# Performance work log

Hardware: AMD Instinct MI355X
Metric: run time of the kernel (lower is better)

## Reference

```python
import jax, jax.numpy as jnp
import numpy as np


def setup_inputs() -> dict:
    key = jax.random.key(0)
    k1, k2, k3, k4 = jax.random.split(key, 4)
    B, C, H, W = 4, 256, 48, 48
    scale = 1.0 / np.sqrt(C)  # conv-like init scale
    x = jax.random.normal(k1, (B, C, H, W), dtype=jnp.float32)
    wq = jax.random.normal(k2, (C, C), dtype=jnp.float32) * scale
    wk = jax.random.normal(k3, (C, C), dtype=jnp.float32) * scale
    wv = jax.random.normal(k4, (C, C), dtype=jnp.float32) * scale
    return {"x": x, "wq": wq, "wk": wk, "wv": wv}


def reference(x, wq, wk, wv):
    B, C, H, W = x.shape
    num_heads = 8
    d_k = C // num_heads
    N = H * W

    # 1x1 convs (bias=False) are channel-mixing matmuls: [out_c, in_c]
    def proj(w):
        y = jnp.einsum('oc,bchw->bohw', w, x)
        # view(B, heads, d_k, H*W)
        return y.reshape(B, num_heads, d_k, N)

    q = proj(wq)  # [B, h, d_k, N]
    k = proj(wk)
    v = proj(wv)

    # scores = q^T k / sqrt(d_k) -> [B, h, N, N]
    scores = jnp.einsum('bhdn,bhdm->bhnm', q, k) / jnp.sqrt(jnp.asarray(d_k, x.dtype))
    attn = jax.nn.softmax(scores, axis=-1)
    # out = attn @ v^T -> [B, h, N, d_k]
    out = jnp.einsum('bhnm,bhdm->bhnd', attn, v)
    # permute back to [B, h, d_k, N] then view(B, C, H, W)
    out = out.transpose(0, 1, 3, 2).reshape(B, C, H, W)
    return x + out
```

## Files before the change

### kernel.cpp

```cpp
#include <hip/hip_runtime.h>

constexpr int B  = 4;
constexpr int C  = 256;
constexpr int N  = 2304;
constexpr int NH = 8;
constexpr int DK = 32;

typedef short short8 __attribute__((ext_vector_type(8)));
typedef float f32x4  __attribute__((ext_vector_type(4)));

static __device__ __forceinline__ ushort f2bf(float f) {
    union { float f; unsigned u; } v; v.f = f;
    return (ushort)((v.u + 0x7FFFu + ((v.u >> 16) & 1u)) >> 16);
}
static __device__ __forceinline__ unsigned cvtpk(float lo, float hi) {
    unsigned r;
    asm("v_cvt_pk_bf16_f32 %0, %1, %2" : "=v"(r) : "v"(lo), "v"(hi));
    return r;
}

__global__ __launch_bounds__(256) void proj_kernel(
    const float* __restrict__ x,
    const float* __restrict__ wq,
    const float* __restrict__ wk,
    const float* __restrict__ wv,
    ushort* __restrict__ ws,
    int bfix, size_t matStride, size_t batchStride)
{
    const int mat = blockIdx.y;
    const int b   = (bfix >= 0) ? bfix : (int)blockIdx.z;
    const int n0  = (blockIdx.x % 18) * 128;
    const int o0  = (blockIdx.x / 18) * 128;

    const float* w = (mat == 0) ? wq : (mat == 1) ? wk : wv;
    ushort* out = ws + (size_t)mat * matStride + (size_t)b * batchStride;
    const float* xb = x + (size_t)b * C * N;

    __shared__ float xs[16][128];
    __shared__ float wtT[16][132];

    const int tid = threadIdx.x;
    const int tx = tid >> 4;
    const int ty = tid & 15;

    float acc[8][8] = {};

    for (int k0 = 0; k0 < C; k0 += 16) {
        {
            const int kk  = tid >> 4;
            const int nn4 = tid & 15;
            *reinterpret_cast<float4*>(&xs[kk][nn4 * 4]) =
                *reinterpret_cast<const float4*>(xb + (size_t)(k0 + kk) * N + n0 + nn4 * 4);
            *reinterpret_cast<float4*>(&xs[kk][64 + nn4 * 4]) =
                *reinterpret_cast<const float4*>(xb + (size_t)(k0 + kk) * N + n0 + 64 + nn4 * 4);
        }
        {
            const int oo = tid >> 1;
            const int kh = tid & 1;
            float4 wa = *reinterpret_cast<const float4*>(w + (size_t)(o0 + oo) * C + k0 + kh * 4);
            float4 wb = *reinterpret_cast<const float4*>(w + (size_t)(o0 + oo) * C + k0 + kh * 4 + 8);
            wtT[kh * 4 + 0][oo] = wa.x;
            wtT[kh * 4 + 1][oo] = wa.y;
            wtT[kh * 4 + 2][oo] = wa.z;
            wtT[kh * 4 + 3][oo] = wa.w;
            wtT[kh * 4 + 8][oo] = wb.x;
            wtT[kh * 4 + 9][oo] = wb.y;
            wtT[kh * 4 + 10][oo] = wb.z;
            wtT[kh * 4 + 11][oo] = wb.w;
        }
        __syncthreads();

        #pragma unroll
        for (int kk = 0; kk < 16; ++kk) {
            float4 a0 = *reinterpret_cast<const float4*>(&xs[kk][tx * 8]);
            float4 a1 = *reinterpret_cast<const float4*>(&xs[kk][tx * 8 + 4]);
            float4 b0 = *reinterpret_cast<const float4*>(&wtT[kk][ty * 8]);
            float4 b1 = *reinterpret_cast<const float4*>(&wtT[kk][ty * 8 + 4]);
            float av[8] = {a0.x, a0.y, a0.z, a0.w, a1.x, a1.y, a1.z, a1.w};
            float bv[8] = {b0.x, b0.y, b0.z, b0.w, b1.x, b1.y, b1.z, b1.w};
            #pragma unroll
            for (int jn = 0; jn < 8; ++jn)
                #pragma unroll
                for (int jo = 0; jo < 8; ++jo)
                    acc[jn][jo] = fmaf(av[jn], bv[jo], acc[jn][jo]);
        }
        __syncthreads();
    }

    const float sc = (mat == 0) ? 0.25503450535f : 1.0f;
    #pragma unroll
    for (int jn = 0; jn < 8; ++jn) {
        unsigned pk[4];
        #pragma unroll
        for (int p = 0; p < 4; ++p)
            pk[p] = cvtpk(acc[jn][2 * p] * sc, acc[jn][2 * p + 1] * sc);
        *reinterpret_cast<uint4*>(out + (size_t)(n0 + tx * 8 + jn) * C + o0 + ty * 8) =
            make_uint4(pk[0], pk[1], pk[2], pk[3]);
    }
}

__global__ __launch_bounds__(128) void attn_kernel(
    const ushort* __restrict__ ws,
    const float* __restrict__ x,
    float* __restrict__ out,
    int bfix, size_t matStride, size_t batchStride, int ppx)
{
    __shared__ __align__(16) char smem[14336];
    ushort* Ks  = (ushort*)smem;
    ushort* Vt  = (ushort*)(smem + 5120);
    float*  Ost = (float*) smem;

    const int tid = threadIdx.x;
    const int wq  = tid >> 6;
    const int l   = tid & 63;
    const int lq  = l & 15;
    const int g   = l >> 4;

    ushort* Pl = (ushort*)(smem + 9728) + wq * 1152;

    const int gid  = blockIdx.x;
    const int xcd  = gid & 7;
    const int loc  = gid >> 3;
    const int pair = xcd * ppx + loc / 72;
    const int qt   = loc % 72;
    const int h    = pair & 7;
    const int b    = (bfix >= 0) ? bfix : (pair >> 3);
    const int n0   = qt * 32;

    const ushort* qb = ws + (size_t)b * batchStride;
    const ushort* kb = qb + matStride;
    const ushort* vb = qb + 2 * matStride;

    short8 qf = *reinterpret_cast<const short8*>(
        qb + (size_t)(n0 + wq * 16 + lq) * C + h * DK + 8 * g);

    f32x4 acc0 = {0.f, 0.f, 0.f, 0.f};
    f32x4 acc1 = {0.f, 0.f, 0.f, 0.f};
    float m = -1e30f, lsum = 0.f;

    const int kr = tid >> 2, kc = tid & 3;
    const int vp = tid & 31, vd = tid >> 5;

    short8  kreg0, kreg1;
    ushort4 va0, vc0, va1, vc1;

    #define LOAD_TILE(m0_)                                                          \
        {                                                                           \
            const int m0i = (m0_);                                                  \
            kreg0 = *reinterpret_cast<const short8*>(kb + (size_t)(m0i + kr) * C + h * DK + kc * 8);        \
            kreg1 = *reinterpret_cast<const short8*>(kb + (size_t)(m0i + 32 + kr) * C + h * DK + kc * 8);   \
            const ushort* v0 = vb + (size_t)(m0i + 2 * vp) * C + h * DK + vd * 4;   \
            va0 = *reinterpret_cast<const ushort4*>(v0);                            \
            vc0 = *reinterpret_cast<const ushort4*>(v0 + C);                        \
            va1 = *reinterpret_cast<const ushort4*>(v0 + 16);                       \
            vc1 = *reinterpret_cast<const ushort4*>(v0 + C + 16);                   \
        }

    LOAD_TILE(0);

    for (int t = 0; t < N / 64; ++t) {
        *reinterpret_cast<short8*>(Ks + kr * 40 + kc * 8) = kreg0;
        *reinterpret_cast<short8*>(Ks + (kr + 32) * 40 + kc * 8) = kreg1;
        {
            unsigned p0 = (unsigned)va0.x | ((unsigned)vc0.x << 16);
            unsigned p1 = (unsigned)va0.y | ((unsigned)vc0.y << 16);
            unsigned p2 = (unsigned)va0.z | ((unsigned)vc0.z << 16);
            unsigned p3 = (unsigned)va0.w | ((unsigned)vc0.w << 16);
            *reinterpret_cast<unsigned*>(Vt + (vd * 4 + 0) * 72 + 2 * vp) = p0;
            *reinterpret_cast<unsigned*>(Vt + (vd * 4 + 1) * 72 + 2 * vp) = p1;
            *reinterpret_cast<unsigned*>(Vt + (vd * 4 + 2) * 72 + 2 * vp) = p2;
            *reinterpret_cast<unsigned*>(Vt + (vd * 4 + 3) * 72 + 2 * vp) = p3;
            unsigned q0 = (unsigned)va1.x | ((unsigned)vc1.x << 16);
            unsigned q1 = (unsigned)va1.y | ((unsigned)vc1.y << 16);
            unsigned q2 = (unsigned)va1.z | ((unsigned)vc1.z << 16);
            unsigned q3 = (unsigned)va1.w | ((unsigned)vc1.w << 16);
            *reinterpret_cast<unsigned*>(Vt + (vd * 4 + 16) * 72 + 2 * vp) = q0;
            *reinterpret_cast<unsigned*>(Vt + (vd * 4 + 17) * 72 + 2 * vp) = q1;
            *reinterpret_cast<unsigned*>(Vt + (vd * 4 + 18) * 72 + 2 * vp) = q2;
            *reinterpret_cast<unsigned*>(Vt + (vd * 4 + 19) * 72 + 2 * vp) = q3;
        }
        __syncthreads();

        if (t < N / 64 - 1) LOAD_TILE((t + 1) * 64);

        f32x4 st[4];
        __builtin_amdgcn_s_setprio(1);
        #pragma unroll
        for (int u = 0; u < 4; ++u) {
            short8 kf = *reinterpret_cast<const short8*>(Ks + (lq + 16 * u) * 40 + 8 * g);
            f32x4 z = {0.f, 0.f, 0.f, 0.f};
            st[u] = __builtin_amdgcn_mfma_f32_16x16x32_bf16(kf, qf, z, 0, 0, 0);
        }
        __builtin_amdgcn_s_setprio(0);

        float mxl = st[0][0];
        #pragma unroll
        for (int u = 0; u < 4; ++u)
            #pragma unroll
            for (int r = 0; r < 4; ++r) mxl = fmaxf(mxl, st[u][r]);

        if (!__all(mxl <= m + 8.0f)) {
            float mx = fmaxf(mxl, __shfl_xor(mxl, 16));
            mx = fmaxf(mx, __shfl_xor(mx, 32));
            float nm = fmaxf(m, mx);
            float corr = exp2f(m - nm);
            m = nm;
            lsum *= corr;
            float cw0 = __shfl(corr, 4 * g + 0);
            float cw1 = __shfl(corr, 4 * g + 1);
            float cw2 = __shfl(corr, 4 * g + 2);
            float cw3 = __shfl(corr, 4 * g + 3);
            acc0[0] *= cw0; acc0[1] *= cw1; acc0[2] *= cw2; acc0[3] *= cw3;
            acc1[0] *= cw0; acc1[1] *= cw1; acc1[2] *= cw2; acc1[3] *= cw3;
        }

        float ps = 0.f;
        uint2 pw[4];
        #pragma unroll
        for (int u = 0; u < 4; ++u) {
            float p0 = exp2f(st[u][0] - m);
            float p1 = exp2f(st[u][1] - m);
            float p2 = exp2f(st[u][2] - m);
            float p3 = exp2f(st[u][3] - m);
            ps += (p0 + p1) + (p2 + p3);
            pw[u].x = cvtpk(p0, p1);
            pw[u].y = cvtpk(p2, p3);
        }
        lsum += ps;

        #pragma unroll
        for (int u = 0; u < 4; ++u)
            *reinterpret_cast<uint2*>(Pl + lq * 72 + 4 * g + 16 * u) = pw[u];

        short8 pf0 = *reinterpret_cast<const short8*>(Pl + lq * 72 + 8 * g);
        short8 pf1 = *reinterpret_cast<const short8*>(Pl + lq * 72 + 32 + 8 * g);
        __builtin_amdgcn_s_setprio(1);
        #pragma unroll
        for (int k2 = 0; k2 < 2; ++k2) {
            short8 pf = k2 ? pf1 : pf0;
            short8 vf0 = *reinterpret_cast<const short8*>(Vt + lq * 72 + 32 * k2 + 8 * g);
            short8 vf1 = *reinterpret_cast<const short8*>(Vt + (lq + 16) * 72 + 32 * k2 + 8 * g);
            acc0 = __builtin_amdgcn_mfma_f32_16x16x32_bf16(pf, vf0, acc0, 0, 0, 0);
            acc1 = __builtin_amdgcn_mfma_f32_16x16x32_bf16(pf, vf1, acc1, 0, 0, 0);
        }
        __builtin_amdgcn_s_setprio(0);
        __syncthreads();
    }

    lsum += __shfl_xor(lsum, 16);
    lsum += __shfl_xor(lsum, 32);
    const float iv = 1.0f / lsum;
    float iw0 = __shfl(iv, 4 * g + 0);
    float iw1 = __shfl(iv, 4 * g + 1);
    float iw2 = __shfl(iv, 4 * g + 2);
    float iw3 = __shfl(iv, 4 * g + 3);

    Ost[(lq +  0) * 36 + wq * 16 + 4 * g + 0] = acc0[0] * iw0;
    Ost[(lq +  0) * 36 + wq * 16 + 4 * g + 1] = acc0[1] * iw1;
    Ost[(lq +  0) * 36 + wq * 16 + 4 * g + 2] = acc0[2] * iw2;
    Ost[(lq +  0) * 36 + wq * 16 + 4 * g + 3] = acc0[3] * iw3;
    Ost[(lq + 16) * 36 + wq * 16 + 4 * g + 0] = acc1[0] * iw0;
    Ost[(lq + 16) * 36 + wq * 16 + 4 * g + 1] = acc1[1] * iw1;
    Ost[(lq + 16) * 36 + wq * 16 + 4 * g + 2] = acc1[2] * iw2;
    Ost[(lq + 16) * 36 + wq * 16 + 4 * g + 3] = acc1[3] * iw3;
    __syncthreads();

    {
        const int d  = tid >> 2;
        const int nn = (tid & 3) * 8;
        const size_t go = ((size_t)b * C + h * DK + d) * (size_t)N + n0 + nn;
        float4 o1 = *reinterpret_cast<float4*>(Ost + d * 36 + nn);
        float4 o2 = *reinterpret_cast<float4*>(Ost + d * 36 + nn + 4);
        float4 x1 = *reinterpret_cast<const float4*>(x + go);
        float4 x2 = *reinterpret_cast<const float4*>(x + go + 4);
        *reinterpret_cast<float4*>(out + go)     = make_float4(o1.x + x1.x, o1.y + x1.y, o1.z + x1.z, o1.w + x1.w);
        *reinterpret_cast<float4*>(out + go + 4) = make_float4(o2.x + x2.x, o2.y + x2.y, o2.z + x2.z, o2.w + x2.w);
    }
}

extern "C" void kernel_launch(void* const* d_in, const int* in_sizes, int n_in,
                              void* d_out, int out_size, void* d_ws, size_t ws_size,
                              hipStream_t stream) {
    const float* x  = (const float*)d_in[0];
    const float* wq = (const float*)d_in[1];
    const float* wk = (const float*)d_in[2];
    const float* wv = (const float*)d_in[3];
    float* out = (float*)d_out;
    ushort* ws = (ushort*)d_ws;

    const size_t NC = (size_t)N * C;
    const size_t needFull = 3 * (size_t)B * NC * sizeof(ushort);

    if (ws_size >= needFull) {
        proj_kernel<<<dim3(18 * 2, 3, B), 256, 0, stream>>>(
            x, wq, wk, wv, ws, -1, (size_t)B * NC, NC);
        attn_kernel<<<dim3(72 * NH * B), 128, 0, stream>>>(
            ws, x, out, -1, (size_t)B * NC, NC, 4);
    } else {
        for (int b = 0; b < B; ++b) {
            proj_kernel<<<dim3(18 * 2, 3, 1), 256, 0, stream>>>(
                x, wq, wk, wv, ws, b, NC, 0);
            attn_kernel<<<dim3(72 * NH), 128, 0, stream>>>(
                ws, x, out, b, NC, 0, 1);
        }
    }
}
```

Measured before the change: 221.3 us.

## Enlarge attention query tile to 128 rows with 8-wave blocks sharing K/V tiles

The attention kernel now runs 512-thread blocks covering 128 queries instead of 128-thread blocks covering 32. Each K/V tile staged in shared memory is therefore reused by four times as many queries, which cuts global and L2 load traffic and per-query staging work. K loading and V loading/transposing are split between the two halves of the block. In exchange, shared memory per block grows, 8-wave barriers are costlier, and the grid shrinks to 576 blocks, which may leave load imbalance across CUs.

```diff
diff --git a/kernel.cpp b/kernel.cpp
--- a/kernel.cpp
+++ b/kernel.cpp
@@ -9,10 +9,6 @@
 typedef short short8 __attribute__((ext_vector_type(8)));
 typedef float f32x4  __attribute__((ext_vector_type(4)));
 
-static __device__ __forceinline__ ushort f2bf(float f) {
-    union { float f; unsigned u; } v; v.f = f;
-    return (ushort)((v.u + 0x7FFFu + ((v.u >> 16) & 1u)) >> 16);
-}
 static __device__ __forceinline__ unsigned cvtpk(float lo, float hi) {
     unsigned r;
     asm("v_cvt_pk_bf16_f32 %0, %1, %2" : "=v"(r) : "v"(lo), "v"(hi));
@@ -99,13 +95,13 @@
     }
 }
 
-__global__ __launch_bounds__(128) void attn_kernel(
+__global__ __launch_bounds__(512) void attn_kernel(
     const ushort* __restrict__ ws,
     const float* __restrict__ x,
     float* __restrict__ out,
     int bfix, size_t matStride, size_t batchStride, int ppx)
 {
-    __shared__ __align__(16) char smem[14336];
+    __shared__ __align__(16) char smem[28160];
     ushort* Ks  = (ushort*)smem;
     ushort* Vt  = (ushort*)(smem + 5120);
     float*  Ost = (float*) smem;
@@ -121,11 +117,11 @@
     const int gid  = blockIdx.x;
     const int xcd  = gid & 7;
     const int loc  = gid >> 3;
-    const int pair = xcd * ppx + loc / 72;
-    const int qt   = loc % 72;
+    const int pair = xcd * ppx + loc / 18;
+    const int qt   = loc % 18;
     const int h    = pair & 7;
     const int b    = (bfix >= 0) ? bfix : (pair >> 3);
-    const int n0   = qt * 32;
+    const int n0   = qt * 128;
 
     const ushort* qb = ws + (size_t)b * batchStride;
     const ushort* kb = qb + matStride;
@@ -139,45 +135,33 @@
     float m = -1e30f, lsum = 0.f;
 
     const int kr = tid >> 2, kc = tid & 3;
-    const int vp = tid & 31, vd = tid >> 5;
-
-    short8  kreg0, kreg1;
-    ushort4 va0, vc0, va1, vc1;
-
-    #define LOAD_TILE(m0_)                                                          \
-        {                                                                           \
-            const int m0i = (m0_);                                                  \
-            kreg0 = *reinterpret_cast<const short8*>(kb + (size_t)(m0i + kr) * C + h * DK + kc * 8);        \
-            kreg1 = *reinterpret_cast<const short8*>(kb + (size_t)(m0i + 32 + kr) * C + h * DK + kc * 8);   \
+    const int t2 = tid - 256;
+    const int vp = t2 & 31, vd = t2 >> 5;
+
+    short8  kreg;
+    ushort4 va, vc;
+
+    #define LOAD_TILE(m0_) {                                                        \
+        const int m0i = (m0_);                                                      \
+        if (tid < 256) {                                                            \
+            kreg = *reinterpret_cast<const short8*>(kb + (size_t)(m0i + kr) * C + h * DK + kc * 8); \
+        } else {                                                                    \
             const ushort* v0 = vb + (size_t)(m0i + 2 * vp) * C + h * DK + vd * 4;   \
-            va0 = *reinterpret_cast<const ushort4*>(v0);                            \
-            vc0 = *reinterpret_cast<const ushort4*>(v0 + C);                        \
-            va1 = *reinterpret_cast<const ushort4*>(v0 + 16);                       \
-            vc1 = *reinterpret_cast<const ushort4*>(v0 + C + 16);                   \
-        }
+            va = *reinterpret_cast<const ushort4*>(v0);                             \
+            vc = *reinterpret_cast<const ushort4*>(v0 + C);                         \
+        }                                                                           \
+    }
 
     LOAD_TILE(0);
 
     for (int t = 0; t < N / 64; ++t) {
-        *reinterpret_cast<short8*>(Ks + kr * 40 + kc * 8) = kreg0;
-        *reinterpret_cast<short8*>(Ks + (kr + 32) * 40 + kc * 8) = kreg1;
-        {
-            unsigned p0 = (unsigned)va0.x | ((unsigned)vc0.x << 16);
-            unsigned p1 = (unsigned)va0.y | ((unsigned)vc0.y << 16);
-            unsigned p2 = (unsigned)va0.z | ((unsigned)vc0.z << 16);
-            unsigned p3 = (unsigned)va0.w | ((unsigned)vc0.w << 16);
-            *reinterpret_cast<unsigned*>(Vt + (vd * 4 + 0) * 72 + 2 * vp) = p0;
-            *reinterpret_cast<unsigned*>(Vt + (vd * 4 + 1) * 72 + 2 * vp) = p1;
-            *reinterpret_cast<unsigned*>(Vt + (vd * 4 + 2) * 72 + 2 * vp) = p2;
-            *reinterpret_cast<unsigned*>(Vt + (vd * 4 + 3) * 72 + 2 * vp) = p3;
-            unsigned q0 = (unsigned)va1.x | ((unsigned)vc1.x << 16);
-            unsigned q1 = (unsigned)va1.y | ((unsigned)vc1.y << 16);
-            unsigned q2 = (unsigned)va1.z | ((unsigned)vc1.z << 16);
-            unsigned q3 = (unsigned)va1.w | ((unsigned)vc1.w << 16);
-            *reinterpret_cast<unsigned*>(Vt + (vd * 4 + 16) * 72 + 2 * vp) = q0;
-            *reinterpret_cast<unsigned*>(Vt + (vd * 4 + 17) * 72 + 2 * vp) = q1;
-            *reinterpret_cast<unsigned*>(Vt + (vd * 4 + 18) * 72 + 2 * vp) = q2;
-            *reinterpret_cast<unsigned*>(Vt + (vd * 4 + 19) * 72 + 2 * vp) = q3;
+        if (tid < 256) {
+            *reinterpret_cast<short8*>(Ks + kr * 40 + kc * 8) = kreg;
+        } else {
+            *reinterpret_cast<unsigned*>(Vt + (vd * 4 + 0) * 72 + 2 * vp) = (unsigned)va.x | ((unsigned)vc.x << 16);
+            *reinterpret_cast<unsigned*>(Vt + (vd * 4 + 1) * 72 + 2 * vp) = (unsigned)va.y | ((unsigned)vc.y << 16);
+            *reinterpret_cast<unsigned*>(Vt + (vd * 4 + 2) * 72 + 2 * vp) = (unsigned)va.z | ((unsigned)vc.z << 16);
+            *reinterpret_cast<unsigned*>(Vt + (vd * 4 + 3) * 72 + 2 * vp) = (unsigned)va.w | ((unsigned)vc.w << 16);
         }
         __syncthreads();
 
@@ -255,22 +239,22 @@
     float iw2 = __shfl(iv, 4 * g + 2);
     float iw3 = __shfl(iv, 4 * g + 3);
 
-    Ost[(lq +  0) * 36 + wq * 16 + 4 * g + 0] = acc0[0] * iw0;
-    Ost[(lq +  0) * 36 + wq * 16 + 4 * g + 1] = acc0[1] * iw1;
-    Ost[(lq +  0) * 36 + wq * 16 + 4 * g + 2] = acc0[2] * iw2;
-    Ost[(lq +  0) * 36 + wq * 16 + 4 * g + 3] = acc0[3] * iw3;
-    Ost[(lq + 16) * 36 + wq * 16 + 4 * g + 0] = acc1[0] * iw0;
-    Ost[(lq + 16) * 36 + wq * 16 + 4 * g + 1] = acc1[1] * iw1;
-    Ost[(lq + 16) * 36 + wq * 16 + 4 * g + 2] = acc1[2] * iw2;
-    Ost[(lq + 16) * 36 + wq * 16 + 4 * g + 3] = acc1[3] * iw3;
+    Ost[(lq +  0) * 132 + wq * 16 + 4 * g + 0] = acc0[0] * iw0;
+    Ost[(lq +  0) * 132 + wq * 16 + 4 * g + 1] = acc0[1] * iw1;
+    Ost[(lq +  0) * 132 + wq * 16 + 4 * g + 2] = acc0[2] * iw2;
+    Ost[(lq +  0) * 132 + wq * 16 + 4 * g + 3] = acc0[3] * iw3;
+    Ost[(lq + 16) * 132 + wq * 16 + 4 * g + 0] = acc1[0] * iw0;
+    Ost[(lq + 16) * 132 + wq * 16 + 4 * g + 1] = acc1[1] * iw1;
+    Ost[(lq + 16) * 132 + wq * 16 + 4 * g + 2] = acc1[2] * iw2;
+    Ost[(lq + 16) * 132 + wq * 16 + 4 * g + 3] = acc1[3] * iw3;
     __syncthreads();
 
     {
-        const int d  = tid >> 2;
-        const int nn = (tid & 3) * 8;
+        const int d  = tid >> 4;
+        const int nn = (tid & 15) * 8;
         const size_t go = ((size_t)b * C + h * DK + d) * (size_t)N + n0 + nn;
-        float4 o1 = *reinterpret_cast<float4*>(Ost + d * 36 + nn);
-        float4 o2 = *reinterpret_cast<float4*>(Ost + d * 36 + nn + 4);
+        float4 o1 = *reinterpret_cast<float4*>(Ost + d * 132 + nn);
+        float4 o2 = *reinterpret_cast<float4*>(Ost + d * 132 + nn + 4);
         float4 x1 = *reinterpret_cast<const float4*>(x + go);
         float4 x2 = *reinterpret_cast<const float4*>(x + go + 4);
         *reinterpret_cast<float4*>(out + go)     = make_float4(o1.x + x1.x, o1.y + x1.y, o1.z + x1.z, o1.w + x1.w);
@@ -294,13 +278,13 @@
     if (ws_size >= needFull) {
         proj_kernel<<<dim3(18 * 2, 3, B), 256, 0, stream>>>(
             x, wq, wk, wv, ws, -1, (size_t)B * NC, NC);
-        attn_kernel<<<dim3(72 * NH * B), 128, 0, stream>>>(
+        attn_kernel<<<dim3(18 * NH * B), 512, 0, stream>>>(
             ws, x, out, -1, (size_t)B * NC, NC, 4);
     } else {
         for (int b = 0; b < B; ++b) {
             proj_kernel<<<dim3(18 * 2, 3, 1), 256, 0, stream>>>(
                 x, wq, wk, wv, ws, b, NC, 0);
-            attn_kernel<<<dim3(72 * NH), 128, 0, stream>>>(
+            attn_kernel<<<dim3(18 * NH), 512, 0, stream>>>(
                 ws, x, out, b, NC, 0, 1);
         }
     }
```

After: 204.4 us. 7.6% less time.
